# Performance work log

Measured on AMD Instinct MI355X. Metric: run time of the kernel, lower is better.

Reference implementation:

```python
import jax, jax.numpy as jnp
import numpy as np

EPS = 1e-12  # torch F.normalize eps


def _row_normalized_gram(f):
    # f: [B, C] -> A = f f^T per sample, rows L2-normalized (dim=1)
    A = jnp.einsum('bi,bj->bij', f, f)                      # [B, C, C]
    n = jnp.sqrt(jnp.sum(A * A, axis=-1, keepdims=True))    # row norms
    return A / jnp.maximum(n, EPS)


def setup_inputs() -> dict:
    key = jax.random.key(0)
    k1, k2 = jax.random.split(key)
    B, C = 32, 2048
    return {
        'feat_src_T': jax.random.normal(k1, (B, C), dtype=jnp.float32),
        'feat_tgt_S': jax.random.normal(k2, (B, C), dtype=jnp.float32),
    }


def reference(feat_src_T, feat_tgt_S):
    B, C = feat_src_T.shape
    d = _row_normalized_gram(feat_src_T) - _row_normalized_gram(feat_tgt_S)
    # torch.norm(d)**2 == sum of squares (Frobenius); divide by C per sample, mean over B
    per_sample = jnp.sum(d * d, axis=(1, 2)) / C            # [B]
    return jnp.mean(per_sample)
```

## Files before the change

### kernel.cpp

```cpp
#include <hip/hip_runtime.h>


constexpr int B = 32;
constexpr int C = 2048;
constexpr int THREADS = 256;

__global__ __launch_bounds__(THREADS) void csl_stage1(const float* __restrict__ x,
                                                      const float* __restrict__ y,
                                                      float* __restrict__ ws) {
    const int b = blockIdx.x;
    const int tid = threadIdx.x;
    const float4* x4 = reinterpret_cast<const float4*>(x + (size_t)b * C);
    const float4* y4 = reinterpret_cast<const float4*>(y + (size_t)b * C);

    float sx2 = 0.f, sy2 = 0.f, sxy = 0.f, sp = 0.f, cx = 0.f, cy = 0.f;
    #pragma unroll
    for (int i = tid; i < C / 4; i += THREADS) {
        const float4 a = x4[i];
        const float4 c4 = y4[i];
        const float av[4] = {a.x, a.y, a.z, a.w};
        const float bv[4] = {c4.x, c4.y, c4.z, c4.w};
        #pragma unroll
        for (int k = 0; k < 4; ++k) {
            const float u = av[k], v = bv[k];
            sx2 = fmaf(u, u, sx2);
            sy2 = fmaf(v, v, sy2);
            sxy = fmaf(u, v, sxy);
            const float su = (u > 0.f) ? 1.f : ((u < 0.f) ? -1.f : 0.f);
            const float sv = (v > 0.f) ? 1.f : ((v < 0.f) ? -1.f : 0.f);
            sp += su * sv;
            cx += (u != 0.f) ? 1.f : 0.f;
            cy += (v != 0.f) ? 1.f : 0.f;
        }
    }

    #pragma unroll
    for (int off = 32; off >= 1; off >>= 1) {
        sx2 += __shfl_down(sx2, off);
        sy2 += __shfl_down(sy2, off);
        sxy += __shfl_down(sxy, off);
        sp  += __shfl_down(sp,  off);
        cx  += __shfl_down(cx,  off);
        cy  += __shfl_down(cy,  off);
    }

    __shared__ float red[6][THREADS / 64];
    const int wave = tid >> 6;
    if ((tid & 63) == 0) {
        red[0][wave] = sx2; red[1][wave] = sy2; red[2][wave] = sxy;
        red[3][wave] = sp;  red[4][wave] = cx;  red[5][wave] = cy;
    }
    __syncthreads();
    if (tid == 0) {
        float t[6];
        #pragma unroll
        for (int j = 0; j < 6; ++j) {
            t[j] = red[j][0];
            #pragma unroll
            for (int w = 1; w < THREADS / 64; ++w) t[j] += red[j][w];
        }
        const float nx = sqrtf(t[0]);
        const float ny = sqrtf(t[1]);
        const float denom = fmaxf(nx * ny, 1e-24f);
        const float cosv = t[2] / denom;
        ws[b] = t[4] + t[5] - 2.f * t[3] * cosv;
    }
}

__global__ __launch_bounds__(64) void csl_stage2(const float* __restrict__ ws,
                                                 float* __restrict__ out) {
    const int tid = threadIdx.x;
    float v = (tid < B) ? ws[tid] : 0.f;
    #pragma unroll
    for (int off = 32; off >= 1; off >>= 1) v += __shfl_down(v, off);
    if (tid == 0) out[0] = v / (float)(B * C);
}

extern "C" void kernel_launch(void* const* d_in, const int* in_sizes, int n_in,
                              void* d_out, int out_size, void* d_ws, size_t ws_size,
                              hipStream_t stream) {
    const float* x = (const float*)d_in[0];
    const float* y = (const float*)d_in[1];
    float* ws = (float*)d_ws;
    csl_stage1<<<B, THREADS, 0, stream>>>(x, y, ws);
    csl_stage2<<<1, 64, 0, stream>>>(ws, (float*)d_out);
}
```

Baseline: 11.29 us.

## Fuse two-stage reduction into a single one-block kernel with per-wave samples

Replaces the two-kernel launch (per-sample block reduction plus a final sum kernel) with one 1024-thread block in which each wave handles two samples and reduces with shuffles only. The final mean is computed in the same block through shared memory, removing the second launch and the workspace round trip. The trade-off is that all 512 KB of input is now streamed by a single block on one CU instead of 32 blocks, which limits memory-level parallelism.

```diff
diff --git a/kernel.cpp b/kernel.cpp
--- a/kernel.cpp
+++ b/kernel.cpp
@@ -3,77 +3,83 @@
 
 constexpr int B = 32;
 constexpr int C = 2048;
-constexpr int THREADS = 256;
+constexpr int THREADS = 1024;
 
-__global__ __launch_bounds__(THREADS) void csl_stage1(const float* __restrict__ x,
+__global__ __launch_bounds__(THREADS) void csl_single(const float* __restrict__ x,
                                                       const float* __restrict__ y,
-                                                      float* __restrict__ ws) {
-    const int b = blockIdx.x;
-    const int tid = threadIdx.x;
-    const float4* x4 = reinterpret_cast<const float4*>(x + (size_t)b * C);
-    const float4* y4 = reinterpret_cast<const float4*>(y + (size_t)b * C);
+                                                      float* __restrict__ out) {
+    const int tid  = threadIdx.x;
+    const int wave = tid >> 6;
+    const int lane = tid & 63;
+    const int s0 = wave * 2;
+    const int s1 = s0 + 1;
 
-    float sx2 = 0.f, sy2 = 0.f, sxy = 0.f, sp = 0.f, cx = 0.f, cy = 0.f;
+    const float4* x40 = reinterpret_cast<const float4*>(x + (size_t)s0 * C);
+    const float4* x41 = reinterpret_cast<const float4*>(x + (size_t)s1 * C);
+    const float4* y40 = reinterpret_cast<const float4*>(y + (size_t)s0 * C);
+    const float4* y41 = reinterpret_cast<const float4*>(y + (size_t)s1 * C);
+
+    float a_sx2 = 0.f, a_sy2 = 0.f, a_sxy = 0.f, a_sp = 0.f, a_cx = 0.f, a_cy = 0.f;
+    float b_sx2 = 0.f, b_sy2 = 0.f, b_sxy = 0.f, b_sp = 0.f, b_cx = 0.f, b_cy = 0.f;
+
+    auto accum = [](float u, float v, float& sx2, float& sy2, float& sxy,
+                    float& sp, float& cx, float& cy) {
+        sx2 = fmaf(u, u, sx2);
+        sy2 = fmaf(v, v, sy2);
+        sxy = fmaf(u, v, sxy);
+        const float su = (u > 0.f) ? 1.f : ((u < 0.f) ? -1.f : 0.f);
+        const float sv = (v > 0.f) ? 1.f : ((v < 0.f) ? -1.f : 0.f);
+        sp += su * sv;
+        cx += (u != 0.f) ? 1.f : 0.f;
+        cy += (v != 0.f) ? 1.f : 0.f;
+    };
+
     #pragma unroll
-    for (int i = tid; i < C / 4; i += THREADS) {
-        const float4 a = x4[i];
-        const float4 c4 = y4[i];
-        const float av[4] = {a.x, a.y, a.z, a.w};
-        const float bv[4] = {c4.x, c4.y, c4.z, c4.w};
-        #pragma unroll
-        for (int k = 0; k < 4; ++k) {
-            const float u = av[k], v = bv[k];
-            sx2 = fmaf(u, u, sx2);
-            sy2 = fmaf(v, v, sy2);
-            sxy = fmaf(u, v, sxy);
-            const float su = (u > 0.f) ? 1.f : ((u < 0.f) ? -1.f : 0.f);
-            const float sv = (v > 0.f) ? 1.f : ((v < 0.f) ? -1.f : 0.f);
-            sp += su * sv;
-            cx += (u != 0.f) ? 1.f : 0.f;
-            cy += (v != 0.f) ? 1.f : 0.f;
-        }
+    for (int j = 0; j < C / 4 / 64; ++j) {
+        const int idx = lane + 64 * j;
+        const float4 xa = x40[idx];
+        const float4 ya = y40[idx];
+        const float4 xb = x41[idx];
+        const float4 yb = y41[idx];
+        accum(xa.x, ya.x, a_sx2, a_sy2, a_sxy, a_sp, a_cx, a_cy);
+        accum(xa.y, ya.y, a_sx2, a_sy2, a_sxy, a_sp, a_cx, a_cy);
+        accum(xa.z, ya.z, a_sx2, a_sy2, a_sxy, a_sp, a_cx, a_cy);
+        accum(xa.w, ya.w, a_sx2, a_sy2, a_sxy, a_sp, a_cx, a_cy);
+        accum(xb.x, yb.x, b_sx2, b_sy2, b_sxy, b_sp, b_cx, b_cy);
+        accum(xb.y, yb.y, b_sx2, b_sy2, b_sxy, b_sp, b_cx, b_cy);
+        accum(xb.z, yb.z, b_sx2, b_sy2, b_sxy, b_sp, b_cx, b_cy);
+        accum(xb.w, yb.w, b_sx2, b_sy2, b_sxy, b_sp, b_cx, b_cy);
     }
 
     #pragma unroll
     for (int off = 32; off >= 1; off >>= 1) {
-        sx2 += __shfl_down(sx2, off);
-        sy2 += __shfl_down(sy2, off);
-        sxy += __shfl_down(sxy, off);
-        sp  += __shfl_down(sp,  off);
-        cx  += __shfl_down(cx,  off);
-        cy  += __shfl_down(cy,  off);
+        a_sx2 += __shfl_down(a_sx2, off);  a_sy2 += __shfl_down(a_sy2, off);
+        a_sxy += __shfl_down(a_sxy, off);  a_sp  += __shfl_down(a_sp,  off);
+        a_cx  += __shfl_down(a_cx,  off);  a_cy  += __shfl_down(a_cy,  off);
+        b_sx2 += __shfl_down(b_sx2, off);  b_sy2 += __shfl_down(b_sy2, off);
+        b_sxy += __shfl_down(b_sxy, off);  b_sp  += __shfl_down(b_sp,  off);
+        b_cx  += __shfl_down(b_cx,  off);  b_cy  += __shfl_down(b_cy,  off);
     }
 
-    __shared__ float red[6][THREADS / 64];
-    const int wave = tid >> 6;
-    if ((tid & 63) == 0) {
-        red[0][wave] = sx2; red[1][wave] = sy2; red[2][wave] = sxy;
-        red[3][wave] = sp;  red[4][wave] = cx;  red[5][wave] = cy;
+    __shared__ float vals[B];
+    if (lane == 0) {
+        {
+            const float denom = fmaxf(sqrtf(a_sx2) * sqrtf(a_sy2), 1e-24f);
+            vals[s0] = a_cx + a_cy - 2.f * a_sp * (a_sxy / denom);
+        }
+        {
+            const float denom = fmaxf(sqrtf(b_sx2) * sqrtf(b_sy2), 1e-24f);
+            vals[s1] = b_cx + b_cy - 2.f * b_sp * (b_sxy / denom);
+        }
     }
     __syncthreads();
-    if (tid == 0) {
-        float t[6];
+
+    if (tid < 64) {
+        float v = (tid < B) ? vals[tid] : 0.f;
         #pragma unroll
-        for (int j = 0; j < 6; ++j) {
-            t[j] = red[j][0];
-            #pragma unroll
-            for (int w = 1; w < THREADS / 64; ++w) t[j] += red[j][w];
-        }
-        const float nx = sqrtf(t[0]);
-        const float ny = sqrtf(t[1]);
-        const float denom = fmaxf(nx * ny, 1e-24f);
-        const float cosv = t[2] / denom;
-        ws[b] = t[4] + t[5] - 2.f * t[3] * cosv;
+        for (int off = 32; off >= 1; off >>= 1) v += __shfl_down(v, off);
+        if (tid == 0) out[0] = v * (1.f / (float)(B * C));
     }
-}
-
-__global__ __launch_bounds__(64) void csl_stage2(const float* __restrict__ ws,
-                                                 float* __restrict__ out) {
-    const int tid = threadIdx.x;
-    float v = (tid < B) ? ws[tid] : 0.f;
-    #pragma unroll
-    for (int off = 32; off >= 1; off >>= 1) v += __shfl_down(v, off);
-    if (tid == 0) out[0] = v / (float)(B * C);
 }
 
 extern "C" void kernel_launch(void* const* d_in, const int* in_sizes, int n_in,
@@ -81,7 +87,5 @@
                               hipStream_t stream) {
     const float* x = (const float*)d_in[0];
     const float* y = (const float*)d_in[1];
-    float* ws = (float*)d_ws;
-    csl_stage1<<<B, THREADS, 0, stream>>>(x, y, ws);
-    csl_stage2<<<1, 64, 0, stream>>>(ws, (float*)d_out);
+    csl_single<<<1, THREADS, 0, stream>>>(x, y, (float*)d_out);
 }
```

Result: slower. 14.21 us (+25.9%).
